# Kernel tuning notes

Hardware: AMD Instinct MI355X
Metric: run time of the kernel (lower is better)

The kernel has to match this reference:

```python
import jax, jax.numpy as jnp
import numpy as np

B, N, DIM = 8, 2048, 1024


def setup_inputs() -> dict:
    key = jax.random.key(0)
    k1, k2 = jax.random.split(key, 2)
    x = jax.random.normal(k1, (B, N, DIM), dtype=jnp.float32)
    # to_qk: Linear(dim, 2*dim), xavier-uniform weight, zero bias
    limit = float(np.sqrt(6.0 / (DIM + 2 * DIM)))
    W_qk = jax.random.uniform(k2, (2 * DIM, DIM), dtype=jnp.float32,
                              minval=-limit, maxval=limit)
    b_qk = jnp.zeros((2 * DIM,), dtype=jnp.float32)
    return {"x": x, "W_qk": W_qk, "b_qk": b_qk}


def reference(x, W_qk, b_qk):
    # x: [b, n, d]; single-head attention, value = raw input x (no V projection).
    b, n, d = x.shape
    qk = x @ W_qk.T + b_qk                      # [b, n, 2d]
    q, k = qk[..., :d], qk[..., d:]             # rearrange 'b n (qk d) -> qk b n d'
    # original: dots = matmul1([k, q^T]) -> dots[b,i,j] = k_i . q_j
    dots = jnp.einsum('bid,bjd->bij', k, q) * (d ** -0.5)
    attn = jax.nn.softmax(dots, axis=-1)        # dropout is identity in eval mode
    out = jnp.einsum('bij,bjd->bid', attn, x)   # value is the cloned input t = x
    return out
```

## Files before the change

### kernel.cpp

```cpp
#include <hip/hip_runtime.h>
#include <hip/hip_bf16.h>
#include <stdint.h>

typedef unsigned short u16;
typedef __attribute__((ext_vector_type(4))) float f32x4;
typedef __attribute__((ext_vector_type(8))) short bf16x8;
typedef __attribute__((ext_vector_type(4))) unsigned short u16x4;
typedef __attribute__((ext_vector_type(8))) unsigned short u16x8;

__device__ inline u16 f2bf(float f) {
    unsigned int u = __builtin_bit_cast(unsigned int, f);
    u = u + 0x7fffu + ((u >> 16) & 1u);
    return (u16)(u >> 16);
}
__device__ inline float bf2f(u16 h) {
    return __builtin_bit_cast(float, ((unsigned int)h) << 16);
}
__device__ inline void gld_lds16(const void* g, void* l) {
    __builtin_amdgcn_global_load_lds((__attribute__((address_space(1))) void*)(g),
                                     (__attribute__((address_space(3))) void*)(l),
                                     16, 0, 0);
}

#define SB0() __builtin_amdgcn_sched_barrier(0)
#define BARRIER() do { __builtin_amdgcn_s_barrier(); SB0(); } while (0)
#define LGKM0()   do { asm volatile("s_waitcnt lgkmcnt(0)" ::: "memory"); SB0(); } while (0)

template <int BF16OUT, int BIAS, int EXPOUT, int RSCALE, int PARTSUM, int DROPBAR>
__global__ __launch_bounds__(512, 2)
void gemm256(const u16* __restrict__ A, const u16* __restrict__ B,
             void* __restrict__ Cv, const float* __restrict__ bias,
             const float* __restrict__ rs, long sRb, float* __restrict__ part,
             int K, int lda, int ldb, int ldc,
             long sAb, long sBb, long sCb, float scale)
{
    __shared__ __align__(16) char lds[131072];

    const int tid  = threadIdx.x;
    const int lane = tid & 63;
    const int w    = tid >> 6;
    const int wm   = w >> 2, wn = w & 3;

    const int gx   = gridDim.x, gy = gridDim.y;
    const int flat = blockIdx.x + gx * (blockIdx.y + gy * blockIdx.z);
    const int nwg  = gx * gy * gridDim.z;
    const int swz  = (flat & 7) * (nwg >> 3) + (flat >> 3);
    const int mt   = swz % gx;
    const int rest = swz / gx;
    const int ntl  = rest % gy;
    const int zb   = rest / gy;

    const u16* Ab = A + (long)zb * sAb;
    const u16* Bb = B + (long)zb * sBb;
    const long rowA0 = (long)mt * 256;
    const long rowB0 = (long)ntl * 256;

    const int srow   = w * 16 + (lane >> 3);
    const int schunk = (lane & 7) ^ ((lane >> 3) & 7);
    const u16* aG = Ab + (rowA0 + srow) * (long)lda + schunk * 8;
    const u16* bG = Bb + (rowB0 + srow) * (long)ldb + schunk * 8;

    const int NT = K >> 6;

    auto stageA = [&](int t, int hh) {
        if (t >= NT) return;
        const u16* s = aG + (long)hh * 128 * lda + (long)t * 64;
        char* d = lds + (t & 1) * 65536 + hh * 16384 + w * 2048;
        gld_lds16(s, d);
        gld_lds16(s + 8 * (long)lda, d + 1024);
    };
    auto stageB = [&](int t, int hh) {
        if (t >= NT) return;
        const u16* s = bG + (long)hh * 128 * ldb + (long)t * 64;
        char* d = lds + (t & 1) * 65536 + 32768 + hh * 16384 + w * 2048;
        gld_lds16(s, d);
        gld_lds16(s + 8 * (long)ldb, d + 1024);
    };

    const int rl    = lane & 15;
    const int kbyte = (lane >> 4) * 16;
    auto ldA = [&](int cur, int m, int kh) -> bf16x8 {
        const int row = wm * 128 + m * 16 + rl;
        const int byt = (kh * 64 + kbyte) ^ ((row & 7) << 4);
        return *(const bf16x8*)(lds + cur * 65536 + row * 128 + byt);
    };
    auto ldB = [&](int cur, int n, int kh) -> bf16x8 {
        const int row = wn * 64 + n * 16 + rl;
        const int byt = (kh * 64 + kbyte) ^ ((row & 7) << 4);
        return *(const bf16x8*)(lds + cur * 65536 + 32768 + row * 128 + byt);
    };

    f32x4 acc[8][4] = {};
    bf16x8 a0[4][2], a1[4][2], b0[2][2], b1[2][2];

    stageA(0, 0); stageA(0, 1);
    stageB(0, 0); stageB(0, 1);
    stageA(1, 0); stageA(1, 1);
    asm volatile("s_waitcnt vmcnt(4)" ::: "memory");
    BARRIER();

    for (int t = 0; t < NT; ++t) {
        const int cur = t & 1;

        stageB(t + 1, 0);
#pragma unroll
        for (int m = 0; m < 4; ++m)
#pragma unroll
            for (int kh = 0; kh < 2; ++kh) a0[m][kh] = ldA(cur, m, kh);
#pragma unroll
        for (int n = 0; n < 2; ++n)
#pragma unroll
            for (int kh = 0; kh < 2; ++kh) b0[n][kh] = ldB(cur, n, kh);
        if (!DROPBAR) BARRIER();
        LGKM0();
        __builtin_amdgcn_s_setprio(1);
#pragma unroll
        for (int kh = 0; kh < 2; ++kh)
#pragma unroll
            for (int m = 0; m < 4; ++m)
#pragma unroll
                for (int n = 0; n < 2; ++n)
                    acc[m][n] = __builtin_amdgcn_mfma_f32_16x16x32_bf16(
                        a0[m][kh], b0[n][kh], acc[m][n], 0, 0, 0);
        __builtin_amdgcn_s_setprio(0);
        BARRIER();

        stageB(t + 1, 1);
#pragma unroll
        for (int m = 0; m < 4; ++m)
#pragma unroll
            for (int kh = 0; kh < 2; ++kh) a1[m][kh] = ldA(cur, m + 4, kh);
        if (!DROPBAR) BARRIER();
        LGKM0();
        __builtin_amdgcn_s_setprio(1);
#pragma unroll
        for (int kh = 0; kh < 2; ++kh)
#pragma unroll
            for (int m = 0; m < 4; ++m)
#pragma unroll
                for (int n = 0; n < 2; ++n)
                    acc[m + 4][n] = __builtin_amdgcn_mfma_f32_16x16x32_bf16(
                        a1[m][kh], b0[n][kh], acc[m + 4][n], 0, 0, 0);
        __builtin_amdgcn_s_setprio(0);
        BARRIER();

        stageA(t + 2, 0);
#pragma unroll
        for (int n = 0; n < 2; ++n)
#pragma unroll
            for (int kh = 0; kh < 2; ++kh) b1[n][kh] = ldB(cur, n + 2, kh);
        if (!DROPBAR) BARRIER();
        LGKM0();
        __builtin_amdgcn_s_setprio(1);
#pragma unroll
        for (int kh = 0; kh < 2; ++kh)
#pragma unroll
            for (int m = 0; m < 4; ++m)
#pragma unroll
                for (int n = 0; n < 2; ++n)
                    acc[m + 4][n + 2] = __builtin_amdgcn_mfma_f32_16x16x32_bf16(
                        a1[m][kh], b1[n][kh], acc[m + 4][n + 2], 0, 0, 0);
        __builtin_amdgcn_s_setprio(0);
        BARRIER();

        stageA(t + 2, 1);
        if (!DROPBAR) BARRIER();
        __builtin_amdgcn_s_setprio(1);
#pragma unroll
        for (int kh = 0; kh < 2; ++kh)
#pragma unroll
            for (int m = 0; m < 4; ++m)
#pragma unroll
                for (int n = 0; n < 2; ++n)
                    acc[m][n + 2] = __builtin_amdgcn_mfma_f32_16x16x32_bf16(
                        a0[m][kh], b1[n][kh], acc[m][n + 2], 0, 0, 0);
        __builtin_amdgcn_s_setprio(0);
        if (t < NT - 2) { asm volatile("s_waitcnt vmcnt(4)" ::: "memory"); }
        else            { asm volatile("s_waitcnt vmcnt(0)" ::: "memory"); }
        SB0();
        BARRIER();
    }

#pragma unroll
    for (int m = 0; m < 8; ++m) {
        const long row0 = rowA0 + wm * 128 + m * 16 + (lane >> 4) * 4;
        float rv[4];
        if (RSCALE) {
#pragma unroll
            for (int j = 0; j < 4; ++j) rv[j] = rs[(long)zb * sRb + row0 + j];
        }
        float rsum[4] = {0.f, 0.f, 0.f, 0.f};
#pragma unroll
        for (int n = 0; n < 4; ++n) {
            const long col = rowB0 + wn * 64 + n * 16 + (lane & 15);
            float bv = 0.0f;
            if (BIAS) bv = bias[col];
#pragma unroll
            for (int j = 0; j < 4; ++j) {
                float val = acc[m][n][j] * scale + bv;
                if (EXPOUT) val = __expf(val);
                if (PARTSUM) rsum[j] += val;
                if (RSCALE) val *= rv[j];
                const long idx = (long)zb * sCb + (row0 + j) * ldc + col;
                if (BF16OUT) ((u16*)Cv)[idx] = f2bf(val);
                else         ((float*)Cv)[idx] = val;
            }
        }
        if (PARTSUM) {
#pragma unroll
            for (int j = 0; j < 4; ++j)
#pragma unroll
                for (int o = 1; o < 16; o <<= 1) rsum[j] += __shfl_xor(rsum[j], o);
            if ((lane & 15) == 0) {
#pragma unroll
                for (int j = 0; j < 4; ++j)
                    part[((long)zb * 2048 + row0 + j) * 32 + ntl * 4 + wn] = rsum[j];
            }
        }
    }
}

__global__ __launch_bounds__(256)
void rowsum_inv(const float* __restrict__ part, float* __restrict__ rs)
{
    const long row = (long)blockIdx.x * 256 + threadIdx.x;
    const f32x4* p = (const f32x4*)(part + row * 32);
    float s = 0.0f;
#pragma unroll
    for (int q = 0; q < 8; ++q) {
        f32x4 v = p[q];
        s += v[0] + v[1] + v[2] + v[3];
    }
    rs[row] = 1.0f / s;
}

__global__ __launch_bounds__(256)
void cvt_bf16(const float* __restrict__ src, u16* __restrict__ dst, long n4)
{
    const long i = (long)blockIdx.x * 256 + threadIdx.x;
    if (i >= n4) return;
    f32x4 v = ((const f32x4*)src)[i];
    u16x4 o;
#pragma unroll
    for (int j = 0; j < 4; ++j) o[j] = f2bf(v[j]);
    ((u16x4*)dst)[i] = o;
}

__global__ __launch_bounds__(256)
void prep_x(const float* __restrict__ x, u16* __restrict__ xb, u16* __restrict__ xT)
{
    __shared__ float tile[32][33];
    const int  b  = blockIdx.z;
    const long n0 = (long)blockIdx.x * 32;
    const long d0 = (long)blockIdx.y * 32;
    const int  t  = threadIdx.x;
    const int  r  = t >> 3;
    const int  c  = (t & 7) * 4;

    f32x4 v = *(const f32x4*)(x + ((long)b * 2048 + n0 + r) * 1024 + d0 + c);
    u16x4 s;
#pragma unroll
    for (int j = 0; j < 4; ++j) { s[j] = f2bf(v[j]); tile[r][c + j] = v[j]; }
    *(u16x4*)(xb + ((long)b * 2048 + n0 + r) * 1024 + d0 + c) = s;
    __syncthreads();

    u16x4 o;
#pragma unroll
    for (int j = 0; j < 4; ++j) o[j] = f2bf(tile[c + j][r]);
    *(u16x4*)(xT + ((long)b * 1024 + d0 + r) * 2048 + n0 + c) = o;
}

extern "C" void kernel_launch(void* const* d_in, const int* in_sizes, int n_in,
                              void* d_out, int out_size, void* d_ws, size_t ws_size,
                              hipStream_t stream)
{
    const float* x   = (const float*)d_in[0];
    const float* Wqk = (const float*)d_in[1];
    const float* bqk = (const float*)d_in[2];
    float* out = (float*)d_out;

    char* ws = (char*)d_ws;
    u16*   xT   = (u16*)(ws);
    u16*   qk   = (u16*)(ws + 33554432L);
    u16*   sc   = (u16*)(ws + 100663296L);
    u16*   xb   = (u16*)(ws + 100663296L);
    u16*   Wb   = (u16*)(ws + 134217728L);
    float* rs   = (float*)(ws + 167772160L);
    float* part = (float*)(ws + 167837696L);

    cvt_bf16<<<2048, 256, 0, stream>>>(Wqk, Wb, 2048L * 1024 / 4);
    prep_x<<<dim3(64, 32, 8), 256, 0, stream>>>(x, xb, xT);

    gemm256<1, 1, 0, 0, 0, 0><<<dim3(64, 8, 1), 512, 0, stream>>>(
        xb, Wb, qk, bqk, nullptr, 0, nullptr,
        1024, 1024, 1024, 2048, 0, 0, 0, 1.0f);

    gemm256<1, 0, 1, 0, 1, 0><<<dim3(8, 8, 8), 512, 0, stream>>>(
        qk + 1024, qk, sc, nullptr, nullptr, 0, part,
        1024, 2048, 2048, 2048,
        2048L * 2048, 2048L * 2048, 2048L * 2048, 0.03125f);

    rowsum_inv<<<64, 256, 0, stream>>>(part, rs);

    gemm256<0, 0, 0, 1, 0, 1><<<dim3(8, 4, 8), 512, 0, stream>>>(
        sc, xT, out, nullptr, rs, 2048, nullptr,
        2048, 2048, 2048, 1024,
        2048L * 2048, 1024L * 2048, 2048L * 1024, 1.0f);
}
```

Measured before the change: 257.9 us.

## Fold Wk·Wqᵀ into one matrix to halve the projection GEMM

Uses softmax row-shift invariance to rewrite k·qᵀ as x·(Wk Wqᵀ)·xᵀ plus a per-column bias term from the key bias. A small kernel precomputes the 1024x1024 product matrix and a bias vector. The projection GEMM then produces only 1024 columns instead of 2048, and the score GEMM consumes y and bf16 x directly. The barrier-dropping variant of the final GEMM is removed. Extra rounding of the fused matrix to bf16 may change accuracy slightly.

```diff
diff --git a/kernel.cpp b/kernel.cpp
--- a/kernel.cpp
+++ b/kernel.cpp
@@ -26,10 +26,10 @@
 #define BARRIER() do { __builtin_amdgcn_s_barrier(); SB0(); } while (0)
 #define LGKM0()   do { asm volatile("s_waitcnt lgkmcnt(0)" ::: "memory"); SB0(); } while (0)
 
-template <int BF16OUT, int BIAS, int EXPOUT, int RSCALE, int PARTSUM, int DROPBAR>
+template <int BF16OUT, int BIAS, int EXPOUT, int RSCALE, int PARTSUM>
 __global__ __launch_bounds__(512, 2)
 void gemm256(const u16* __restrict__ A, const u16* __restrict__ B,
-             void* __restrict__ Cv, const float* __restrict__ bias,
+             void* __restrict__ Cv, const float* __restrict__ bias, long sBias,
              const float* __restrict__ rs, long sRb, float* __restrict__ part,
              int K, int lda, int ldb, int ldc,
              long sAb, long sBb, long sCb, float scale)
@@ -111,7 +111,7 @@
         for (int n = 0; n < 2; ++n)
 #pragma unroll
             for (int kh = 0; kh < 2; ++kh) b0[n][kh] = ldB(cur, n, kh);
-        if (!DROPBAR) BARRIER();
+        BARRIER();
         LGKM0();
         __builtin_amdgcn_s_setprio(1);
 #pragma unroll
@@ -130,7 +130,7 @@
         for (int m = 0; m < 4; ++m)
 #pragma unroll
             for (int kh = 0; kh < 2; ++kh) a1[m][kh] = ldA(cur, m + 4, kh);
-        if (!DROPBAR) BARRIER();
+        BARRIER();
         LGKM0();
         __builtin_amdgcn_s_setprio(1);
 #pragma unroll
@@ -149,7 +149,7 @@
         for (int n = 0; n < 2; ++n)
 #pragma unroll
             for (int kh = 0; kh < 2; ++kh) b1[n][kh] = ldB(cur, n + 2, kh);
-        if (!DROPBAR) BARRIER();
+        BARRIER();
         LGKM0();
         __builtin_amdgcn_s_setprio(1);
 #pragma unroll
@@ -164,7 +164,7 @@
         BARRIER();
 
         stageA(t + 2, 1);
-        if (!DROPBAR) BARRIER();
+        BARRIER();
         __builtin_amdgcn_s_setprio(1);
 #pragma unroll
         for (int kh = 0; kh < 2; ++kh)
@@ -194,7 +194,7 @@
         for (int n = 0; n < 4; ++n) {
             const long col = rowB0 + wn * 64 + n * 16 + (lane & 15);
             float bv = 0.0f;
-            if (BIAS) bv = bias[col];
+            if (BIAS) bv = bias[(long)zb * sBias + col];
 #pragma unroll
             for (int j = 0; j < 4; ++j) {
                 float val = acc[m][n][j] * scale + bv;
@@ -221,6 +221,97 @@
 }
 
 __global__ __launch_bounds__(256)
+void mt_kernel(const u16* __restrict__ Wt, u16* __restrict__ Mt)
+{
+    __shared__ __align__(16) u16 shA[64 * 64];
+    __shared__ __align__(16) u16 shB[64 * 64];
+    const int tid  = threadIdx.x;
+    const int lane = tid & 63;
+    const int w    = tid >> 6;
+    const int wm   = w >> 1, wn = w & 1;
+    const long rowA0 = (long)blockIdx.x * 64;
+    const long rowB0 = (long)blockIdx.y * 64;
+
+    const int srow   = w * 8 + (lane >> 3);
+    const int schunk = (lane & 7) ^ ((lane >> 3) & 7);
+    const u16* aG = Wt + (rowA0 + srow) * 2048L + schunk * 8;
+    const u16* bG = Wt + (rowB0 + srow) * 2048L + 1024 + schunk * 8;
+
+    const int rl    = lane & 15;
+    const int kbyte = (lane >> 4) * 16;
+    f32x4 acc[2][2] = {};
+
+    for (int t = 0; t < 16; ++t) {
+        gld_lds16(aG + t * 64,              (char*)shA + w * 1024);
+        gld_lds16(aG + t * 64 + 32 * 2048L, (char*)shA + w * 1024 + 4096);
+        gld_lds16(bG + t * 64,              (char*)shB + w * 1024);
+        gld_lds16(bG + t * 64 + 32 * 2048L, (char*)shB + w * 1024 + 4096);
+        asm volatile("s_waitcnt vmcnt(0)" ::: "memory");
+        BARRIER();
+#pragma unroll
+        for (int kh = 0; kh < 2; ++kh) {
+#pragma unroll
+            for (int m = 0; m < 2; ++m) {
+                const int rowa = wm * 32 + m * 16 + rl;
+                const int byta = (kh * 64 + kbyte) ^ ((rowa & 7) << 4);
+                bf16x8 av = *(const bf16x8*)((char*)shA + rowa * 128 + byta);
+#pragma unroll
+                for (int n = 0; n < 2; ++n) {
+                    const int rowb = wn * 32 + n * 16 + rl;
+                    const int bytb = (kh * 64 + kbyte) ^ ((rowb & 7) << 4);
+                    bf16x8 bv = *(const bf16x8*)((char*)shB + rowb * 128 + bytb);
+                    acc[m][n] = __builtin_amdgcn_mfma_f32_16x16x32_bf16(
+                        av, bv, acc[m][n], 0, 0, 0);
+                }
+            }
+        }
+        BARRIER();
+    }
+
+#pragma unroll
+    for (int m = 0; m < 2; ++m)
+#pragma unroll
+        for (int n = 0; n < 2; ++n) {
+            const long row0 = rowA0 + wm * 32 + m * 16 + (lane >> 4) * 4;
+            const long col  = rowB0 + wn * 32 + n * 16 + (lane & 15);
+#pragma unroll
+            for (int j = 0; j < 4; ++j)
+                Mt[(row0 + j) * 1024 + col] = f2bf(acc[m][n][j] * 0.03125f);
+        }
+}
+
+__global__ __launch_bounds__(256)
+void v_kernel(const float* __restrict__ W, const float* __restrict__ b,
+              float* __restrict__ v)
+{
+    const int c = blockIdx.x * 256 + threadIdx.x;
+    float s = 0.0f;
+    for (int o = 0; o < 1024; ++o) s += W[(long)o * 1024 + c] * b[1024 + o];
+    v[c] = s * 0.03125f;
+}
+
+__global__ __launch_bounds__(256)
+void beta_kernel(const u16* __restrict__ xb, const float* __restrict__ v,
+                 float* __restrict__ beta)
+{
+    const int w    = threadIdx.x >> 6;
+    const int lane = threadIdx.x & 63;
+    const long r   = (long)blockIdx.x * 4 + w;
+    const u16x8* p = (const u16x8*)(xb + r * 1024 + lane * 16);
+    u16x8 va = p[0], vb = p[1];
+    const f32x4* q = (const f32x4*)(v + lane * 16);
+    float s = 0.0f;
+#pragma unroll
+    for (int j = 0; j < 8; ++j) {
+        s += bf2f(va[j]) * ((const float*)q)[j];
+        s += bf2f(vb[j]) * ((const float*)q)[8 + j];
+    }
+#pragma unroll
+    for (int o = 32; o; o >>= 1) s += __shfl_xor(s, o);
+    if (lane == 0) beta[r] = s;
+}
+
+__global__ __launch_bounds__(256)
 void rowsum_inv(const float* __restrict__ part, float* __restrict__ rs)
 {
     const long row = (long)blockIdx.x * 256 + threadIdx.x;
@@ -235,15 +326,24 @@
 }
 
 __global__ __launch_bounds__(256)
-void cvt_bf16(const float* __restrict__ src, u16* __restrict__ dst, long n4)
-{
-    const long i = (long)blockIdx.x * 256 + threadIdx.x;
-    if (i >= n4) return;
-    f32x4 v = ((const f32x4*)src)[i];
+void wt_kernel(const float* __restrict__ W, u16* __restrict__ Wt)
+{
+    __shared__ float tile[32][33];
+    const long o0 = (long)blockIdx.x * 32;
+    const long d0 = (long)blockIdx.y * 32;
+    const int  t  = threadIdx.x;
+    const int  r  = t >> 3;
+    const int  c  = (t & 7) * 4;
+
+    f32x4 v = *(const f32x4*)(W + (o0 + r) * 1024 + d0 + c);
+#pragma unroll
+    for (int j = 0; j < 4; ++j) tile[r][c + j] = v[j];
+    __syncthreads();
+
     u16x4 o;
 #pragma unroll
-    for (int j = 0; j < 4; ++j) o[j] = f2bf(v[j]);
-    ((u16x4*)dst)[i] = o;
+    for (int j = 0; j < 4; ++j) o[j] = f2bf(tile[c + j][r]);
+    *(u16x4*)(Wt + (d0 + r) * 2048 + o0 + c) = o;
 }
 
 __global__ __launch_bounds__(256)
@@ -281,29 +381,35 @@
 
     char* ws = (char*)d_ws;
     u16*   xT   = (u16*)(ws);
-    u16*   qk   = (u16*)(ws + 33554432L);
+    u16*   xb   = (u16*)(ws + 33554432L);
+    u16*   y    = (u16*)(ws + 67108864L);
     u16*   sc   = (u16*)(ws + 100663296L);
-    u16*   xb   = (u16*)(ws + 100663296L);
-    u16*   Wb   = (u16*)(ws + 134217728L);
-    float* rs   = (float*)(ws + 167772160L);
-    float* part = (float*)(ws + 167837696L);
-
-    cvt_bf16<<<2048, 256, 0, stream>>>(Wqk, Wb, 2048L * 1024 / 4);
+    u16*   Wt   = (u16*)(ws + 100663296L);
+    u16*   Mt   = (u16*)(ws + 100663296L + 4194304L);
+    float* part = (float*)(ws + 167772160L);
+    float* rs   = (float*)(ws + 169869312L);
+    float* beta = (float*)(ws + 169934848L);
+    float* v    = (float*)(ws + 170000384L);
+
     prep_x<<<dim3(64, 32, 8), 256, 0, stream>>>(x, xb, xT);
-
-    gemm256<1, 1, 0, 0, 0, 0><<<dim3(64, 8, 1), 512, 0, stream>>>(
-        xb, Wb, qk, bqk, nullptr, 0, nullptr,
-        1024, 1024, 1024, 2048, 0, 0, 0, 1.0f);
-
-    gemm256<1, 0, 1, 0, 1, 0><<<dim3(8, 8, 8), 512, 0, stream>>>(
-        qk + 1024, qk, sc, nullptr, nullptr, 0, part,
-        1024, 2048, 2048, 2048,
-        2048L * 2048, 2048L * 2048, 2048L * 2048, 0.03125f);
+    wt_kernel<<<dim3(64, 32), 256, 0, stream>>>(Wqk, Wt);
+    mt_kernel<<<dim3(16, 16), 256, 0, stream>>>(Wt, Mt);
+    v_kernel<<<4, 256, 0, stream>>>(Wqk, bqk, v);
+    beta_kernel<<<4096, 256, 0, stream>>>(xb, v, beta);
+
+    gemm256<1, 0, 0, 0, 0><<<dim3(64, 4, 1), 512, 0, stream>>>(
+        xb, Mt, y, nullptr, 0, nullptr, 0, nullptr,
+        1024, 1024, 1024, 1024, 0, 0, 0, 1.0f);
+
+    gemm256<1, 1, 1, 0, 1><<<dim3(8, 8, 8), 512, 0, stream>>>(
+        y, xb, sc, beta, 2048, nullptr, 0, part,
+        1024, 1024, 1024, 2048,
+        2048L * 1024, 2048L * 1024, 2048L * 2048, 1.0f);
 
     rowsum_inv<<<64, 256, 0, stream>>>(part, rs);
 
-    gemm256<0, 0, 0, 1, 0, 1><<<dim3(8, 4, 8), 512, 0, stream>>>(
-        sc, xT, out, nullptr, rs, 2048, nullptr,
+    gemm256<0, 0, 0, 1, 0><<<dim3(8, 4, 8), 512, 0, stream>>>(
+        sc, xT, out, nullptr, 0, rs, 2048, nullptr,
         2048, 2048, 2048, 1024,
         2048L * 2048, 1024L * 2048, 2048L * 1024, 1.0f);
 }
```

Result: slower. 266.7 us (+3.4%).
